# Performance work log

Measured on AMD Instinct MI355X. Metric: run time of the kernel, lower is better.

## Reference

```python
import jax, jax.numpy as jnp
from jax import lax
import numpy as np

B, T, I, H, O = 512, 2048, 8, 128, 96


def setup_inputs() -> dict:
    key = jax.random.key(0)
    ks = jax.random.split(key, 7)
    s = 1.0 / np.sqrt(H)  # PyTorch GRU init scale
    return {
        "x": jax.random.normal(ks[0], (B, T, I), dtype=jnp.float32),
        "w_ih": jax.random.uniform(ks[1], (3 * H, I), jnp.float32, -s, s),
        "w_hh": jax.random.uniform(ks[2], (3 * H, H), jnp.float32, -s, s),
        "b_ih": jax.random.uniform(ks[3], (3 * H,), jnp.float32, -s, s),
        "b_hh": jax.random.uniform(ks[4], (3 * H,), jnp.float32, -s, s),
        "fc_w": jax.random.uniform(ks[5], (O, H), jnp.float32, -s, s),
        "fc_b": jax.random.uniform(ks[6], (O,), jnp.float32, -s, s),
    }


def reference(x, w_ih, w_hh, b_ih, b_hh, fc_w, fc_b):
    # x: [B, T, I]; PyTorch GRU gate order: reset, update, new (r, z, n)
    Bh, Th, _ = x.shape
    Hh = w_hh.shape[1]
    # Precompute input contributions for all timesteps in one big GEMM.
    gx_all = jnp.einsum('bti,gi->btg', x, w_ih) + b_ih      # [B, T, 3H]
    gx_all = jnp.swapaxes(gx_all, 0, 1)                     # [T, B, 3H]

    def step(h, gx):
        gh = h @ w_hh.T + b_hh                              # [B, 3H]
        r = jax.nn.sigmoid(gx[:, :Hh] + gh[:, :Hh])
        z = jax.nn.sigmoid(gx[:, Hh:2 * Hh] + gh[:, Hh:2 * Hh])
        n = jnp.tanh(gx[:, 2 * Hh:] + r * gh[:, 2 * Hh:])
        h_new = (1.0 - z) * n + z * h
        return h_new, None

    h0 = jnp.zeros((Bh, Hh), x.dtype)
    h_last, _ = lax.scan(step, h0, gx_all)                  # h at final timestep
    return h_last @ fc_w.T + fc_b                           # [B, O]
```

## Files before the change

kernel.cpp:

```cpp
#include <hip/hip_runtime.h>

#define BB 512
#define TT 2048
#define II 8
#define HH 128
#define OO 96

typedef __attribute__((ext_vector_type(8))) short bf16x8;
typedef __attribute__((ext_vector_type(4))) float f32x4;

#define L2E 1.4426950408889634f

__device__ __forceinline__ float fast_rcp(float x) { return __builtin_amdgcn_rcpf(x); }
__device__ __forceinline__ float exp2_fast(float x) {
#if __has_builtin(__builtin_amdgcn_exp2f)
    return __builtin_amdgcn_exp2f(x);
#else
    return __expf(x * 0.6931471805599453f);
#endif
}
__device__ __forceinline__ unsigned short f2bf(float f) {
    unsigned int u = __builtin_bit_cast(unsigned int, f);
    u += 0x7fffu + ((u >> 16) & 1u);
    return (unsigned short)(u >> 16);
}
__device__ __forceinline__ float bf2f(unsigned short h) {
    unsigned int u = ((unsigned int)h) << 16;
    return __builtin_bit_cast(float, u);
}
__device__ __forceinline__ float dot8(const float w[8], float4 a, float4 b, float acc) {
    acc = fmaf(w[0], a.x, acc); acc = fmaf(w[1], a.y, acc);
    acc = fmaf(w[2], a.z, acc); acc = fmaf(w[3], a.w, acc);
    acc = fmaf(w[4], b.x, acc); acc = fmaf(w[5], b.y, acc);
    acc = fmaf(w[6], b.z, acc); acc = fmaf(w[7], b.w, acc);
    return acc;
}

__global__ __launch_bounds__(512, 2) void gru_kernel(
    const float* __restrict__ x,
    const float* __restrict__ w_ih,
    const float* __restrict__ w_hh,
    const float* __restrict__ b_ih,
    const float* __restrict__ b_hh,
    const float* __restrict__ fc_w,
    const float* __restrict__ fc_b,
    float* __restrict__ out)
{
    __shared__ __align__(16) char hbuf[2 * 1280];
    __shared__ __align__(16) float hfin[2][HH];

    const int tid = threadIdx.x;
    const int wv  = tid >> 6;
    const int ln  = tid & 63;
    const int col = ln & 15;
    const int g4  = ln >> 4;
    const int b   = g4 & 1;
    const int sel = (ln >= 32);
    const int p   = ((ln >> 2) & 1) * 2 + (ln & 1);
    const int j   = 16 * wv + col;
    const int b0  = blockIdx.x * 2;

    auto ldfrag_hh = [&](int grow, int ks, float sc) {
        const float* rowp = w_hh + grow * HH + 32 * ks + g4 * 8;
        float4 u = *(const float4*)(rowp);
        float4 v = *(const float4*)(rowp + 4);
        bf16x8 f;
        f[0] = (short)f2bf(sc * u.x); f[1] = (short)f2bf(sc * u.y);
        f[2] = (short)f2bf(sc * u.z); f[3] = (short)f2bf(sc * u.w);
        f[4] = (short)f2bf(sc * v.x); f[5] = (short)f2bf(sc * v.y);
        f[6] = (short)f2bf(sc * v.z); f[7] = (short)f2bf(sc * v.w);
        return f;
    };

    bf16x8 bR[4], bZ[4], bN[4];
#pragma unroll
    for (int ks = 0; ks < 4; ++ks) {
        bR[ks] = ldfrag_hh(j, ks, -L2E);
        bZ[ks] = ldfrag_hh(HH + j, ks, -L2E);
        bN[ks] = ldfrag_hh(2 * HH + j, ks, 2.0f * L2E);
    }

    const int rz_row = sel ? (HH + j) : j;
    float wrz[8], wn[8];
    {
        const float* rzp = w_ih + rz_row * II;
        const float* r2p = w_ih + (2 * HH + j) * II;
#pragma unroll
        for (int i = 0; i < 8; ++i) {
            wrz[i] = -L2E * rzp[i];
            wn[i]  = (2.0f * L2E) * r2p[i];
        }
    }

    const float bias_rz2 = -L2E * (b_ih[rz_row] + b_hh[rz_row]);
    const float bias_nh2 = (2.0f * L2E) * b_hh[2 * HH + j];
    const float bias_nx2 = (2.0f * L2E) * b_ih[2 * HH + j];

    for (int i = tid; i < 640; i += 512) ((int*)hbuf)[i] = 0;
    __syncthreads();

    const char* abase = hbuf + p * 320 + g4 * 16;
    char* wbase = hbuf + b * 640 + (j << 1);
    const float* xp = x + (size_t)(b0 + b) * TT * II;

    float h0 = 0.f;
    const f32x4 zf = {0.f, 0.f, 0.f, 0.f};

    float grz0, gn0, grz1, gn1;
    {
        float4 xa = *(const float4*)(xp);          float4 xb = *(const float4*)(xp + 4);
        float4 xc = *(const float4*)(xp + II);     float4 xd = *(const float4*)(xp + II + 4);
        grz0 = dot8(wrz, xa, xb, bias_rz2);  gn0 = dot8(wn, xa, xb, bias_nx2);
        grz1 = dot8(wrz, xc, xd, bias_rz2);  gn1 = dot8(wn, xc, xd, bias_nx2);
    }
    float grz0n, gn0n, grz1n, gn1n;

#define MFMA_BF16 __builtin_amdgcn_mfma_f32_16x16x32_bf16

#define STEP(RBUF, GRZ, GXN, DOTS)                                              \
    {                                                                           \
        const char* ab = abase + (RBUF) * 1280;                                 \
        bf16x8 a0 = *(const bf16x8*)(ab);                                       \
        bf16x8 a1 = *(const bf16x8*)(ab + 64);                                  \
        bf16x8 a2 = *(const bf16x8*)(ab + 128);                                 \
        bf16x8 a3 = *(const bf16x8*)(ab + 192);                                 \
        f32x4 aR = MFMA_BF16(a0, bR[0], zf, 0, 0, 0);                           \
        f32x4 aZ = MFMA_BF16(a0, bZ[0], zf, 0, 0, 0);                           \
        f32x4 aN = MFMA_BF16(a0, bN[0], zf, 0, 0, 0);                           \
        aR = MFMA_BF16(a1, bR[1], aR, 0, 0, 0);                                 \
        aZ = MFMA_BF16(a1, bZ[1], aZ, 0, 0, 0);                                 \
        aN = MFMA_BF16(a1, bN[1], aN, 0, 0, 0);                                 \
        aR = MFMA_BF16(a2, bR[2], aR, 0, 0, 0);                                 \
        aZ = MFMA_BF16(a2, bZ[2], aZ, 0, 0, 0);                                 \
        aN = MFMA_BF16(a2, bN[2], aN, 0, 0, 0);                                 \
        aR = MFMA_BF16(a3, bR[3], aR, 0, 0, 0);                                 \
        aZ = MFMA_BF16(a3, bZ[3], aZ, 0, 0, 0);                                 \
        aN = MFMA_BF16(a3, bN[3], aN, 0, 0, 0);                                 \
        DOTS                                                                    \
        float c0 = sel ? aZ[0] : aR[0];                                         \
        float c1 = sel ? aZ[1] : aR[1];                                         \
        float grz = c0 + c1 + (GRZ);                                            \
        float s0v = fast_rcp(1.0f + exp2_fast(grz));       \
        float zz  = __shfl_xor(s0v, 32, 64);                 \
        float gn  = aN[0] + aN[1] + bias_nh2;                                   \
        float t0  = fast_rcp(1.0f + exp2_fast(fmaf(s0v, gn, (GXN))));           \
        float n0  = fmaf(-2.0f, t0, 1.0f);                                      \
        h0 = fmaf(zz, h0 - n0, n0);                      \
        if (ln < 32) {                                                          \
            char* w_ = wbase + (1 - (RBUF)) * 1280;                             \
            unsigned short s0 = f2bf(h0);                                       \
            *(unsigned short*)(w_)       = s0;                                  \
            *(unsigned short*)(w_ + 320) = f2bf(h0 - bf2f(s0));                 \
        }                                                                       \
        __syncthreads();                                                        \
    }

    for (int it = 0; it < TT / 2; ++it) {
        int t2 = 2 * it + 2; if (t2 > TT - 1) t2 = TT - 1;
        int t3 = t2 + 1;     if (t3 > TT - 1) t3 = TT - 1;
        float4 pa = *(const float4*)(xp + (size_t)t2 * II);
        float4 pb = *(const float4*)(xp + (size_t)t2 * II + 4);
        float4 pc = *(const float4*)(xp + (size_t)t3 * II);
        float4 pd = *(const float4*)(xp + (size_t)t3 * II + 4);

        STEP(0, grz0, gn0, {
            grz0n = dot8(wrz, pa, pb, bias_rz2);
            gn0n  = dot8(wn,  pa, pb, bias_nx2);
        })
        STEP(1, grz1, gn1, {
            grz1n = dot8(wrz, pc, pd, bias_rz2);
            gn1n  = dot8(wn,  pc, pd, bias_nx2);
        })
        grz0 = grz0n; gn0 = gn0n;
        grz1 = grz1n; gn1 = gn1n;
    }
#undef STEP
#undef MFMA_BF16

    if (ln < 32) hfin[b][j] = h0;
    __syncthreads();

    if (tid < 2 * OO) {
        const int bb2 = (tid >= OO) ? 1 : 0;
        const int o   = tid - OO * bb2;
        const float4* hf = (const float4*)(&hfin[bb2][0]);
        const float4* wp = (const float4*)(fc_w + o * HH);
        float acc = fc_b[o];
#pragma unroll 8
        for (int v = 0; v < HH / 4; ++v) {
            float4 w4 = wp[v];
            float4 h4 = hf[v];
            acc = fmaf(w4.x, h4.x, acc); acc = fmaf(w4.y, h4.y, acc);
            acc = fmaf(w4.z, h4.z, acc); acc = fmaf(w4.w, h4.w, acc);
        }
        out[(size_t)(b0 + bb2) * OO + o] = acc;
    }
}

extern "C" void kernel_launch(void* const* d_in, const int* in_sizes, int n_in,
                              void* d_out, int out_size, void* d_ws, size_t ws_size,
                              hipStream_t stream) {
    const float* x    = (const float*)d_in[0];
    const float* w_ih = (const float*)d_in[1];
    const float* w_hh = (const float*)d_in[2];
    const float* b_ih = (const float*)d_in[3];
    const float* b_hh = (const float*)d_in[4];
    const float* fc_w = (const float*)d_in[5];
    const float* fc_b = (const float*)d_in[6];
    float* out = (float*)d_out;

    gru_kernel<<<BB / 2, 512, 0, stream>>>(x, w_ih, w_hh, b_ih, b_hh, fc_w, fc_b, out);
}
```

Baseline: 884.7 us.

## Process one batch row per block with 4 waves each covering two column tiles

The kernel now runs one batch element per 256-thread block instead of two per 512-thread block. Each wave computes two 16-column tiles of the hidden state (6 MFMA chains instead of 3), and lanes are remapped so the r/z exchange uses a shuffle distance of 16. This doubles the grid to 512 blocks and halves the threads per barrier, which is meant to cut sync cost and improve distribution across CUs. The price is more MFMA work per wave per step, since the M dimension is now mostly padding for a single batch row, plus higher register pressure from 24 B fragments.

New measurement: 1.319 ms. 1.49x slower.

```diff
diff --git a/kernel.cpp b/kernel.cpp
--- a/kernel.cpp
+++ b/kernel.cpp
@@ -36,7 +36,7 @@
     return acc;
 }
 
-__global__ __launch_bounds__(512, 2) void gru_kernel(
+__global__ __launch_bounds__(256, 2) void gru_kernel(
     const float* __restrict__ x,
     const float* __restrict__ w_ih,
     const float* __restrict__ w_hh,
@@ -46,19 +46,21 @@
     const float* __restrict__ fc_b,
     float* __restrict__ out)
 {
-    __shared__ __align__(16) char hbuf[2 * 1280];
-    __shared__ __align__(16) float hfin[2][HH];
-
-    const int tid = threadIdx.x;
-    const int wv  = tid >> 6;
-    const int ln  = tid & 63;
-    const int col = ln & 15;
-    const int g4  = ln >> 4;
-    const int b   = g4 & 1;
-    const int sel = (ln >= 32);
-    const int p   = ((ln >> 2) & 1) * 2 + (ln & 1);
-    const int j   = 16 * wv + col;
-    const int b0  = blockIdx.x * 2;
+    __shared__ __align__(16) char hbuf[2 * 640];
+    __shared__ __align__(16) float hfin[HH];
+
+    const int tid  = threadIdx.x;
+    const int wv   = tid >> 6;
+    const int ln   = tid & 63;
+    const int col  = ln & 15;
+    const int g4   = ln >> 4;
+    const int blkB = g4 >> 1;
+    const int sel  = g4 & 1;
+    const int p    = ln & 1;
+    const int jA   = 32 * wv + col;
+    const int jB   = jA + 16;
+    const int jS   = 32 * wv + 16 * blkB + col;
+    const int b0   = blockIdx.x;
 
     auto ldfrag_hh = [&](int grow, int ks, float sc) {
         const float* rowp = w_hh + grow * HH + 32 * ks + g4 * 8;
@@ -72,19 +74,22 @@
         return f;
     };
 
-    bf16x8 bR[4], bZ[4], bN[4];
+    bf16x8 bRA[4], bZA[4], bNA[4], bRB[4], bZB[4], bNB[4];
 #pragma unroll
     for (int ks = 0; ks < 4; ++ks) {
-        bR[ks] = ldfrag_hh(j, ks, -L2E);
-        bZ[ks] = ldfrag_hh(HH + j, ks, -L2E);
-        bN[ks] = ldfrag_hh(2 * HH + j, ks, 2.0f * L2E);
-    }
-
-    const int rz_row = sel ? (HH + j) : j;
+        bRA[ks] = ldfrag_hh(jA, ks, -L2E);
+        bZA[ks] = ldfrag_hh(HH + jA, ks, -L2E);
+        bNA[ks] = ldfrag_hh(2 * HH + jA, ks, 2.0f * L2E);
+        bRB[ks] = ldfrag_hh(jB, ks, -L2E);
+        bZB[ks] = ldfrag_hh(HH + jB, ks, -L2E);
+        bNB[ks] = ldfrag_hh(2 * HH + jB, ks, 2.0f * L2E);
+    }
+
+    const int rz_row = sel ? (HH + jS) : jS;
     float wrz[8], wn[8];
     {
         const float* rzp = w_ih + rz_row * II;
-        const float* r2p = w_ih + (2 * HH + j) * II;
+        const float* r2p = w_ih + (2 * HH + jS) * II;
 #pragma unroll
         for (int i = 0; i < 8; ++i) {
             wrz[i] = -L2E * rzp[i];
@@ -93,15 +98,15 @@
     }
 
     const float bias_rz2 = -L2E * (b_ih[rz_row] + b_hh[rz_row]);
-    const float bias_nh2 = (2.0f * L2E) * b_hh[2 * HH + j];
-    const float bias_nx2 = (2.0f * L2E) * b_ih[2 * HH + j];
-
-    for (int i = tid; i < 640; i += 512) ((int*)hbuf)[i] = 0;
+    const float bias_nh2 = (2.0f * L2E) * b_hh[2 * HH + jS];
+    const float bias_nx2 = (2.0f * L2E) * b_ih[2 * HH + jS];
+
+    for (int i = tid; i < 320; i += 256) ((int*)hbuf)[i] = 0;
     __syncthreads();
 
     const char* abase = hbuf + p * 320 + g4 * 16;
-    char* wbase = hbuf + b * 640 + (j << 1);
-    const float* xp = x + (size_t)(b0 + b) * TT * II;
+    char* wbase = hbuf + (jS << 1);
+    const float* xp = x + (size_t)b0 * TT * II;
 
     float h0 = 0.f;
     const f32x4 zf = {0.f, 0.f, 0.f, 0.f};
@@ -119,35 +124,49 @@
 
 #define STEP(RBUF, GRZ, GXN, DOTS)                                              \
     {                                                                           \
-        const char* ab = abase + (RBUF) * 1280;                                 \
+        const char* ab = abase + (RBUF) * 640;                                  \
         bf16x8 a0 = *(const bf16x8*)(ab);                                       \
         bf16x8 a1 = *(const bf16x8*)(ab + 64);                                  \
         bf16x8 a2 = *(const bf16x8*)(ab + 128);                                 \
         bf16x8 a3 = *(const bf16x8*)(ab + 192);                                 \
-        f32x4 aR = MFMA_BF16(a0, bR[0], zf, 0, 0, 0);                           \
-        f32x4 aZ = MFMA_BF16(a0, bZ[0], zf, 0, 0, 0);                           \
-        f32x4 aN = MFMA_BF16(a0, bN[0], zf, 0, 0, 0);                           \
-        aR = MFMA_BF16(a1, bR[1], aR, 0, 0, 0);                                 \
-        aZ = MFMA_BF16(a1, bZ[1], aZ, 0, 0, 0);                                 \
-        aN = MFMA_BF16(a1, bN[1], aN, 0, 0, 0);                                 \
-        aR = MFMA_BF16(a2, bR[2], aR, 0, 0, 0);                                 \
-        aZ = MFMA_BF16(a2, bZ[2], aZ, 0, 0, 0);                                 \
-        aN = MFMA_BF16(a2, bN[2], aN, 0, 0, 0);                                 \
-        aR = MFMA_BF16(a3, bR[3], aR, 0, 0, 0);                                 \
-        aZ = MFMA_BF16(a3, bZ[3], aZ, 0, 0, 0);                                 \
-        aN = MFMA_BF16(a3, bN[3], aN, 0, 0, 0);                                 \
+        f32x4 aRA = MFMA_BF16(a0, bRA[0], zf, 0, 0, 0);                         \
+        f32x4 aZA = MFMA_BF16(a0, bZA[0], zf, 0, 0, 0);                         \
+        f32x4 aNA = MFMA_BF16(a0, bNA[0], zf, 0, 0, 0);                         \
+        f32x4 aRB = MFMA_BF16(a0, bRB[0], zf, 0, 0, 0);                         \
+        f32x4 aZB = MFMA_BF16(a0, bZB[0], zf, 0, 0, 0);                         \
+        f32x4 aNB = MFMA_BF16(a0, bNB[0], zf, 0, 0, 0);                         \
+        aRA = MFMA_BF16(a1, bRA[1], aRA, 0, 0, 0);                              \
+        aZA = MFMA_BF16(a1, bZA[1], aZA, 0, 0, 0);                              \
+        aNA = MFMA_BF16(a1, bNA[1], aNA, 0, 0, 0);                              \
+        aRB = MFMA_BF16(a1, bRB[1], aRB, 0, 0, 0);                              \
+        aZB = MFMA_BF16(a1, bZB[1], aZB, 0, 0, 0);                              \
+        aNB = MFMA_BF16(a1, bNB[1], aNB, 0, 0, 0);                              \
+        aRA = MFMA_BF16(a2, bRA[2], aRA, 0, 0, 0);                              \
+        aZA = MFMA_BF16(a2, bZA[2], aZA, 0, 0, 0);                              \
+        aNA = MFMA_BF16(a2, bNA[2], aNA, 0, 0, 0);                              \
+        aRB = MFMA_BF16(a2, bRB[2], aRB, 0, 0, 0);                              \
+        aZB = MFMA_BF16(a2, bZB[2], aZB, 0, 0, 0);                              \
+        aNB = MFMA_BF16(a2, bNB[2], aNB, 0, 0, 0);                              \
+        aRA = MFMA_BF16(a3, bRA[3], aRA, 0, 0, 0);                              \
+        aZA = MFMA_BF16(a3, bZA[3], aZA, 0, 0, 0);                              \
+        aNA = MFMA_BF16(a3, bNA[3], aNA, 0, 0, 0);                              \
+        aRB = MFMA_BF16(a3, bRB[3], aRB, 0, 0, 0);                              \
+        aZB = MFMA_BF16(a3, bZB[3], aZB, 0, 0, 0);                              \
+        aNB = MFMA_BF16(a3, bNB[3], aNB, 0, 0, 0);                              \
         DOTS                                                                    \
-        float c0 = sel ? aZ[0] : aR[0];                                         \
-        float c1 = sel ? aZ[1] : aR[1];                                         \
+        float cr0 = blkB ? aRB[0] : aRA[0],  cr1 = blkB ? aRB[1] : aRA[1];      \
+        float cz0 = blkB ? aZB[0] : aZA[0],  cz1 = blkB ? aZB[1] : aZA[1];      \
+        float cn0 = blkB ? aNB[0] : aNA[0],  cn1 = blkB ? aNB[1] : aNA[1];      \
+        float c0 = sel ? cz0 : cr0,          c1 = sel ? cz1 : cr1;              \
         float grz = c0 + c1 + (GRZ);                                            \
-        float s0v = fast_rcp(1.0f + exp2_fast(grz));       \
-        float zz  = __shfl_xor(s0v, 32, 64);                 \
-        float gn  = aN[0] + aN[1] + bias_nh2;                                   \
+        float s0v = fast_rcp(1.0f + exp2_fast(grz));   \
+        float zz  = __shfl_xor(s0v, 16, 64);               \
+        float gn  = cn0 + cn1 + bias_nh2;                                       \
         float t0  = fast_rcp(1.0f + exp2_fast(fmaf(s0v, gn, (GXN))));           \
         float n0  = fmaf(-2.0f, t0, 1.0f);                                      \
-        h0 = fmaf(zz, h0 - n0, n0);                      \
-        if (ln < 32) {                                                          \
-            char* w_ = wbase + (1 - (RBUF)) * 1280;                             \
+        h0 = fmaf(zz, h0 - n0, n0);                    \
+        if (sel == 0) {                                                         \
+            char* w_ = wbase + (1 - (RBUF)) * 640;                              \
             unsigned short s0 = f2bf(h0);                                       \
             *(unsigned short*)(w_)       = s0;                                  \
             *(unsigned short*)(w_ + 320) = f2bf(h0 - bf2f(s0));                 \
@@ -177,15 +196,13 @@
 #undef STEP
 #undef MFMA_BF16
 
-    if (ln < 32) hfin[b][j] = h0;
+    if (sel == 0) hfin[jS] = h0;
     __syncthreads();
 
-    if (tid < 2 * OO) {
-        const int bb2 = (tid >= OO) ? 1 : 0;
-        const int o   = tid - OO * bb2;
-        const float4* hf = (const float4*)(&hfin[bb2][0]);
-        const float4* wp = (const float4*)(fc_w + o * HH);
-        float acc = fc_b[o];
+    if (tid < OO) {
+        const float4* hf = (const float4*)(&hfin[0]);
+        const float4* wp = (const float4*)(fc_w + tid * HH);
+        float acc = fc_b[tid];
 #pragma unroll 8
         for (int v = 0; v < HH / 4; ++v) {
             float4 w4 = wp[v];
@@ -193,7 +210,7 @@
             acc = fmaf(w4.x, h4.x, acc); acc = fmaf(w4.y, h4.y, acc);
             acc = fmaf(w4.z, h4.z, acc); acc = fmaf(w4.w, h4.w, acc);
         }
-        out[(size_t)(b0 + bb2) * OO + o] = acc;
+        out[(size_t)b0 * OO + tid] = acc;
     }
 }
 
@@ -209,5 +226,5 @@
     const float* fc_b = (const float*)d_in[6];
     float* out = (float*)d_out;
 
-    gru_kernel<<<BB / 2, 512, 0, stream>>>(x, w_ih, w_hh, b_ih, b_hh, fc_w, fc_b, out);
-}
+    gru_kernel<<<BB, 256, 0, stream>>>(x, w_ih, w_hh, b_ih, b_hh, fc_w, fc_b, out);
+}
```
